# Kernel optimization log

Measured on AMD Instinct MI355X. Metric: run time of the kernel, lower is better.

The kernel has to match this reference:

```python
import jax, jax.numpy as jnp
import numpy as np


def setup_inputs() -> dict:
    key = jax.random.key(0)
    ks = jax.random.split(key, 9)
    B, Q, K, F, C = 16, 2048, 2048, 128, 2
    q = jax.random.normal(ks[0], (B, Q, F), dtype=jnp.float32)
    k = jax.random.normal(ks[1], (B, K, F), dtype=jnp.float32)
    v = jax.random.normal(ks[2], (B, K, F), dtype=jnp.float32)
    coords_q = jax.random.uniform(ks[3], (B, Q, C), dtype=jnp.float32)
    coords_k = jax.random.uniform(ks[4], (B, K, C), dtype=jnp.float32)
    attn_mask = jax.random.randint(ks[5], (B, Q, K), 0, 2).astype(jnp.bool_)
    alibi_mask = jax.random.randint(ks[6], (B, Q, K), 0, 2).astype(jnp.bool_)
    bias_scale = jax.random.uniform(ks[7], (1,), dtype=jnp.float32)  # nn.Parameter(torch.rand(1))
    running_mean = jnp.ones((1,), dtype=jnp.float32)  # RunningMeanScaler buffer (eval mode)
    return {"q": q, "k": k, "v": v, "coords_q": coords_q, "coords_k": coords_k,
            "attn_mask": attn_mask, "alibi_mask": alibi_mask,
            "bias_scale": bias_scale, "running_mean": running_mean}


def reference(q, k, v, coords_q, coords_k, attn_mask, alibi_mask, bias_scale, running_mean):
    # [b,q,k] attention logits
    scale = jnp.asarray(k.shape[-1], q.dtype) ** -0.5
    weight_logits = jnp.einsum('bqf,bkf->bqk', q, k) * scale
    # pairwise coordinate distances [b,q,k]
    diff = coords_q[:, :, None, :] - coords_k[:, None, :, :]
    distances = jnp.sqrt(jnp.sum(diff * diff, axis=-1))
    scaled_distances = (distances / running_mean) * bias_scale  # broadcast scalars
    masked_distances = jnp.where(alibi_mask, jnp.zeros((), distances.dtype), scaled_distances)
    weights = jax.nn.softmax(weight_logits, axis=-1)
    masked = jnp.where(attn_mask, jnp.zeros((), weights.dtype), weights - masked_distances)
    attention = jnp.einsum('bqk,bkf->bqf', masked, v)
    return attention
```

## Files before the change

kernel.cpp:

```cpp
#include <hip/hip_runtime.h>
#include <stdint.h>

#define B_  16
#define QL  2048
#define KL  2048
#define FD  128
#define BQ  64
#define BK  32
#define NSTEP (KL/BK)

#define KSTR  136
#define VTOFF 4352
#define VTSTR 36
#define BUFS  8960
#define WS_HALF (B_*KL*FD)

typedef __attribute__((ext_vector_type(8))) short bf16x8;
typedef __attribute__((ext_vector_type(4))) float f32x4;
typedef __attribute__((ext_vector_type(4))) int   i32x4;
typedef __attribute__((ext_vector_type(4))) unsigned int u32x4;

__device__ __forceinline__ unsigned short f2b(float f) {
  union { float f; unsigned u; } x; x.f = f;
  return (unsigned short)((x.u + 0x8000u) >> 16);
}

__device__ __forceinline__ unsigned cvt_pk_bf16(float lo, float hi) {
  unsigned r;
  asm("v_cvt_pk_bf16_f32 %0, %1, %2" : "=v"(r) : "v"(lo), "v"(hi));
  return r;
}

__global__ __launch_bounds__(256) void conv_k(const float* __restrict__ kp,
                                              unsigned short* __restrict__ kb) {
  int idx = (blockIdx.x * 256 + threadIdx.x) * 4;
  float4 u = *(const float4*)(kp + idx);
  ushort4 s4; s4.x = f2b(u.x); s4.y = f2b(u.y); s4.z = f2b(u.z); s4.w = f2b(u.w);
  *(ushort4*)(kb + idx) = s4;
}

__global__ __launch_bounds__(256) void conv_vt(const float* __restrict__ vp,
                                               unsigned short* __restrict__ vt) {
  __shared__ float tl[32 * 132];
  const int t = threadIdx.x, b = blockIdx.x >> 6, kt = blockIdx.x & 63;
  const int r = t >> 3, f0 = (t & 7) * 16;
  const float* src = vp + ((long long)(b * KL + kt * 32 + r)) * FD + f0;
  #pragma unroll
  for (int i = 0; i < 4; ++i)
    *(float4*)&tl[r * 132 + f0 + 4 * i] = *(const float4*)(src + 4 * i);
  __syncthreads();
  const int f = t >> 1, half = t & 1;
  bf16x8 o0, o1;
  #pragma unroll
  for (int j = 0; j < 8; ++j)  o0[j] = (short)f2b(tl[(half * 16 + j) * 132 + f]);
  #pragma unroll
  for (int j = 0; j < 8; ++j)  o1[j] = (short)f2b(tl[(half * 16 + 8 + j) * 132 + f]);
  unsigned short* dst = vt + ((long long)((b * 64 + kt) * FD + f)) * 32 + half * 16;
  *(bf16x8*)dst = o0;
  *(bf16x8*)(dst + 8) = o1;
}

__global__ __launch_bounds__(256, 2) void alibi_attn(
    const unsigned short* __restrict__ kbp,
    const unsigned short* __restrict__ vtp,
    const float* __restrict__ qp,
    const float* __restrict__ cqp,
    const float* __restrict__ ckp,
    const int* __restrict__ amp,
    const int* __restrict__ almp,
    const float* __restrict__ bsp,
    const float* __restrict__ rmp,
    float* __restrict__ outp)
{
  __shared__ unsigned short kv[2 * BUFS];

  const int t    = threadIdx.x;
  const int w    = t >> 6;
  const int lane = t & 63;
  const int l15  = lane & 15;
  const int q4   = lane >> 4;

  const int bid  = blockIdx.x;
  const int xcd  = bid & 7, slot = bid >> 3;
  const int b    = (xcd << 1) | (slot >> 5);
  const int qbase = (slot & 31) * BQ;

  const float bscale = bsp[0] / rmp[0];
  const float sl2 = 0.08838834764831845f * 1.44269504089f;

  const int kr_st = t >> 3, kc_st = (t & 7) * 16;
  const int vf_st = t >> 1, vh_st = (t & 1) * 16;

  {
    const float* qg = qp + ((long long)(b * QL + qbase)) * FD;
    #pragma unroll
    for (int i = 0; i < 8; ++i) {
      int idx = t + 256 * i;
      float4 u = ((const float4*)qg)[idx];
      int row = idx >> 5, col = (idx & 31) * 4;
      ushort4 s4; s4.x = f2b(u.x); s4.y = f2b(u.y); s4.z = f2b(u.z); s4.w = f2b(u.w);
      *(ushort4*)&kv[row * KSTR + col] = s4;
    }
  }
  __syncthreads();
  bf16x8 qfrag[4];
  {
    const int m = w * 16 + l15;
    #pragma unroll
    for (int fs = 0; fs < 4; ++fs)
      qfrag[fs] = *(const bf16x8*)&kv[m * KSTR + fs * 32 + q4 * 8];
  }
  const int qrow = qbase + w * 16 + l15;
  float cqx, cqy;
  {
    float2 c2 = *(const float2*)(cqp + ((long long)(b * QL + qrow)) * 2);
    cqx = c2.x; cqy = c2.y;
  }
  const long long mrow = (long long)(b * QL + qrow) * KL;
  __syncthreads();

  const unsigned short* kgb = kbp + (long long)b * KL * FD;
  const unsigned short* vgb = vtp + (long long)b * KL * FD;

  i32x4 amv[2][2], alv[2][2];
  f32x4 ckf[2][2][2];
  bf16x8 kreg[2][2], vreg[2][2];
  const int klane0 = 4 * q4;
  #pragma unroll
  for (int s = 0; s < 2; ++s) {
    const int k0 = s * 16 + klane0;
    amv[0][s] = __builtin_nontemporal_load((const i32x4*)(amp + mrow + k0));
    alv[0][s] = __builtin_nontemporal_load((const i32x4*)(almp + mrow + k0));
    ckf[0][s][0] = *(const f32x4*)(ckp + ((long long)(b * KL + k0)) * 2);
    ckf[0][s][1] = *(const f32x4*)(ckp + ((long long)(b * KL + k0)) * 2 + 4);
  }
  {
    bf16x8 k0l = *(const bf16x8*)(kgb + kr_st * FD + kc_st);
    bf16x8 k1l = *(const bf16x8*)(kgb + kr_st * FD + kc_st + 8);
    bf16x8 v0l = *(const bf16x8*)(vgb + t * 16);
    bf16x8 v1l = *(const bf16x8*)(vgb + t * 16 + 8);
    *(bf16x8*)&kv[kr_st * KSTR + kc_st]     = k0l;
    *(bf16x8*)&kv[kr_st * KSTR + kc_st + 8] = k1l;
    *(bf16x8*)&kv[VTOFF + vf_st * VTSTR + vh_st]     = v0l;
    *(bf16x8*)&kv[VTOFF + vf_st * VTSTR + vh_st + 8] = v1l;
    kreg[1][0] = *(const bf16x8*)(kgb + (BK + kr_st) * FD + kc_st);
    kreg[1][1] = *(const bf16x8*)(kgb + (BK + kr_st) * FD + kc_st + 8);
    vreg[1][0] = *(const bf16x8*)(vgb + BK * FD + t * 16);
    vreg[1][1] = *(const bf16x8*)(vgb + BK * FD + t * 16 + 8);
  }
  __syncthreads();

  f32x4 O1[8], O2[8];
  #pragma unroll
  for (int n = 0; n < 8; ++n) {
    O1[n] = (f32x4){0.f, 0.f, 0.f, 0.f};
    O2[n] = (f32x4){0.f, 0.f, 0.f, 0.f};
  }
  float lsum = 0.f;

  const int srcA = l15 + ((q4 & 1) << 5);
  const int srcB = srcA + 16;
  const bool lowhalf = (q4 < 2);

  #pragma unroll 2
  for (int kt = 0; kt < NSTEP; ++kt) {
    const int cur = kt & 1, nxt = cur ^ 1;
    const unsigned short* kb = kv + cur * BUFS;
    unsigned short*       nb = kv + nxt * BUFS;

    const int ktf = (kt + 2 < NSTEP) ? (kt + 2) : (NSTEP - 1);
    kreg[cur][0] = *(const bf16x8*)(kgb + (ktf * BK + kr_st) * FD + kc_st);
    kreg[cur][1] = *(const bf16x8*)(kgb + (ktf * BK + kr_st) * FD + kc_st + 8);
    vreg[cur][0] = *(const bf16x8*)(vgb + ktf * (BK * FD) + t * 16);
    vreg[cur][1] = *(const bf16x8*)(vgb + ktf * (BK * FD) + t * 16 + 8);

    const int ktm = (kt + 1 < NSTEP) ? (kt + 1) : kt;
    #pragma unroll
    for (int s = 0; s < 2; ++s) {
      const int kg = ktm * BK + s * 16 + klane0;
      amv[nxt][s] = __builtin_nontemporal_load((const i32x4*)(amp + mrow + kg));
      alv[nxt][s] = __builtin_nontemporal_load((const i32x4*)(almp + mrow + kg));
      ckf[nxt][s][0] = *(const f32x4*)(ckp + ((long long)(b * KL + kg)) * 2);
      ckf[nxt][s][1] = *(const f32x4*)(ckp + ((long long)(b * KL + kg)) * 2 + 4);
    }

    f32x4 S0 = (f32x4){0.f, 0.f, 0.f, 0.f};
    f32x4 S1 = (f32x4){0.f, 0.f, 0.f, 0.f};
    #pragma unroll
    for (int fs = 0; fs < 4; ++fs) {
      bf16x8 kb0 = *(const bf16x8*)&kb[(l15)      * KSTR + fs * 32 + q4 * 8];
      bf16x8 kb1 = *(const bf16x8*)&kb[(16 + l15) * KSTR + fs * 32 + q4 * 8];
      S0 = __builtin_amdgcn_mfma_f32_16x16x32_bf16(kb0, qfrag[fs], S0, 0, 0, 0);
      S1 = __builtin_amdgcn_mfma_f32_16x16x32_bf16(kb1, qfrag[fs], S1, 0, 0, 0);
    }

    float wvv[2][4], tvv[2][4];
    #pragma unroll
    for (int s = 0; s < 2; ++s) {
      const f32x4 Sv = s ? S1 : S0;
      #pragma unroll
      for (int r = 0; r < 4; ++r) {
        float e = __builtin_amdgcn_exp2f(Sv[r] * sl2);
        lsum += e;
        const float ckx = ckf[cur][s][r >> 1][(r & 1) * 2];
        const float cky = ckf[cur][s][r >> 1][(r & 1) * 2 + 1];
        float dx = cqx - ckx, dy = cqy - cky;
        float d  = sqrtf(fmaf(dx, dx, dy * dy)) * bscale;
        int am = amv[cur][s][r], al = alv[cur][s][r];
        wvv[s][r] = am ? 0.f : e;
        tvv[s][r] = (am | al) ? 0.f : d;
      }
    }

    unsigned aX0 = cvt_pk_bf16(wvv[0][0], wvv[0][1]);
    unsigned aX1 = cvt_pk_bf16(wvv[0][2], wvv[0][3]);
    unsigned aX2 = cvt_pk_bf16(wvv[1][0], wvv[1][1]);
    unsigned aX3 = cvt_pk_bf16(wvv[1][2], wvv[1][3]);
    unsigned tX0 = cvt_pk_bf16(tvv[0][0], tvv[0][1]);
    unsigned tX1 = cvt_pk_bf16(tvv[0][2], tvv[0][3]);
    unsigned tX2 = cvt_pk_bf16(tvv[1][0], tvv[1][1]);
    unsigned tX3 = cvt_pk_bf16(tvv[1][2], tvv[1][3]);

    u32x4 wa, ta;
    {
      int y0, y2;
      y0 = __shfl((int)aX0, srcA); y2 = __shfl((int)aX2, srcA);
      wa[0] = (unsigned)(lowhalf ? y0 : y2);
      y0 = __shfl((int)aX1, srcA); y2 = __shfl((int)aX3, srcA);
      wa[1] = (unsigned)(lowhalf ? y0 : y2);
      y0 = __shfl((int)aX0, srcB); y2 = __shfl((int)aX2, srcB);
      wa[2] = (unsigned)(lowhalf ? y0 : y2);
      y0 = __shfl((int)aX1, srcB); y2 = __shfl((int)aX3, srcB);
      wa[3] = (unsigned)(lowhalf ? y0 : y2);
      y0 = __shfl((int)tX0, srcA); y2 = __shfl((int)tX2, srcA);
      ta[0] = (unsigned)(lowhalf ? y0 : y2);
      y0 = __shfl((int)tX1, srcA); y2 = __shfl((int)tX3, srcA);
      ta[1] = (unsigned)(lowhalf ? y0 : y2);
      y0 = __shfl((int)tX0, srcB); y2 = __shfl((int)tX2, srcB);
      ta[2] = (unsigned)(lowhalf ? y0 : y2);
      y0 = __shfl((int)tX1, srcB); y2 = __shfl((int)tX3, srcB);
      ta[3] = (unsigned)(lowhalf ? y0 : y2);
    }
    bf16x8 aw = __builtin_bit_cast(bf16x8, wa);
    bf16x8 at = __builtin_bit_cast(bf16x8, ta);

    #pragma unroll
    for (int n = 0; n < 8; ++n) {
      bf16x8 vb = *(const bf16x8*)&kb[VTOFF + (n * 16 + l15) * VTSTR + q4 * 8];
      O1[n] = __builtin_amdgcn_mfma_f32_16x16x32_bf16(aw, vb, O1[n], 0, 0, 0);
      O2[n] = __builtin_amdgcn_mfma_f32_16x16x32_bf16(at, vb, O2[n], 0, 0, 0);
    }

    *(bf16x8*)&nb[kr_st * KSTR + kc_st]     = kreg[nxt][0];
    *(bf16x8*)&nb[kr_st * KSTR + kc_st + 8] = kreg[nxt][1];
    *(bf16x8*)&nb[VTOFF + vf_st * VTSTR + vh_st]     = vreg[nxt][0];
    *(bf16x8*)&nb[VTOFF + vf_st * VTSTR + vh_st + 8] = vreg[nxt][1];

    asm volatile("s_waitcnt lgkmcnt(0)\n\ts_barrier" ::: "memory");
  }

  lsum += __shfl_xor(lsum, 16, 64);
  lsum += __shfl_xor(lsum, 32, 64);
  float linv[4];
  #pragma unroll
  for (int r = 0; r < 4; ++r) linv[r] = 1.0f / __shfl(lsum, q4 * 4 + r, 64);

  #pragma unroll
  for (int n = 0; n < 8; ++n) {
    #pragma unroll
    for (int r = 0; r < 4; ++r) {
      const int qg_ = qbase + w * 16 + q4 * 4 + r;
      const int f   = n * 16 + l15;
      float val = O1[n][r] * linv[r] - O2[n][r];
      __builtin_nontemporal_store(val, outp + ((long long)(b * QL + qg_)) * FD + f);
    }
  }
}

extern "C" void kernel_launch(void* const* d_in, const int* in_sizes, int n_in,
                              void* d_out, int out_size, void* d_ws, size_t ws_size,
                              hipStream_t stream) {
  const float* q   = (const float*)d_in[0];
  const float* k   = (const float*)d_in[1];
  const float* v   = (const float*)d_in[2];
  const float* cq  = (const float*)d_in[3];
  const float* ck  = (const float*)d_in[4];
  const int*   am  = (const int*)d_in[5];
  const int*   alm = (const int*)d_in[6];
  const float* bs  = (const float*)d_in[7];
  const float* rm  = (const float*)d_in[8];
  float*       out = (float*)d_out;

  unsigned short* kb = (unsigned short*)d_ws;
  unsigned short* vt = kb + WS_HALF;

  hipLaunchKernelGGL(conv_k,  dim3(WS_HALF / 1024), dim3(256), 0, stream, k, kb);
  hipLaunchKernelGGL(conv_vt, dim3(B_ * 64),        dim3(256), 0, stream, v, vt);

  dim3 grid(B_ * (QL / BQ));
  dim3 block(256);
  hipLaunchKernelGGL(alibi_attn, grid, block, 0, stream,
                     kb, vt, q, cq, ck, am, alm, bs, rm, out);
}
```

Measured before the change: 676.0 us.

## Split attention kernel into producer and consumer warps with LDS handoff

Doubles the block to 512 threads. Four producer waves load K/V tiles and masks, compute the masked distance bias tiles, and pack the attn mask into bit words, passing everything through LDS. Four consumer waves only run the MFMAs, exp and softmax accumulation. This is meant to take the global loads and distance math off the MFMA waves' critical path. In exchange it adds LDS traffic and barrier coupling between the two roles, and occupancy may drop with 512-thread blocks.

```diff
diff --git a/kernel.cpp b/kernel.cpp
--- a/kernel.cpp
+++ b/kernel.cpp
@@ -60,7 +60,7 @@
   *(bf16x8*)(dst + 8) = o1;
 }
 
-__global__ __launch_bounds__(256, 2) void alibi_attn(
+__global__ __launch_bounds__(512, 2) void alibi_attn(
     const unsigned short* __restrict__ kbp,
     const unsigned short* __restrict__ vtp,
     const float* __restrict__ qp,
@@ -73,25 +73,78 @@
     float* __restrict__ outp)
 {
   __shared__ unsigned short kv[2 * BUFS];
+  __shared__ u32x4 t_lds[2][256];
+  __shared__ unsigned amw_lds[2][64];
 
   const int t    = threadIdx.x;
-  const int w    = t >> 6;
   const int lane = t & 63;
   const int l15  = lane & 15;
   const int q4   = lane >> 4;
+  const bool is_prod = (t >= 256);
 
   const int bid  = blockIdx.x;
   const int xcd  = bid & 7, slot = bid >> 3;
   const int b    = (xcd << 1) | (slot >> 5);
   const int qbase = (slot & 31) * BQ;
 
+  const float sl2 = 0.08838834764831845f * 1.44269504089f;
+
+  const unsigned short* kgb = kbp + (long long)b * KL * FD;
+  const unsigned short* vgb = vtp + (long long)b * KL * FD;
+
+  const int tp = t & 255;
+  const int kr_st = tp >> 3, kc_st = (tp & 7) * 16;
+  const int vf_st = tp >> 1, vh_st = (tp & 1) * 16;
+  const int pw = (t >> 6) & 3;
+  const int mrow16 = lane >> 2, moct = lane & 3;
+  const long long mrowP = (long long)(b * QL + qbase + pw * 16 + mrow16) * KL;
+  const int qrowT = qbase + pw * 16 + l15;
   const float bscale = bsp[0] / rmp[0];
-  const float sl2 = 0.08838834764831845f * 1.44269504089f;
-
-  const int kr_st = t >> 3, kc_st = (t & 7) * 16;
-  const int vf_st = t >> 1, vh_st = (t & 1) * 16;
-
-  {
+  float cqxP = 0.f, cqyP = 0.f;
+
+  i32x4 am0[2], am1[2], al0[2], al1[2];
+  bf16x8 krg[2], vrg[2];
+
+  auto produce = [&](int sC, int sl, int tile) {
+    unsigned am8 = 0, ob8 = 0;
+    #pragma unroll
+    for (int j = 0; j < 4; ++j) {
+      am8 |= (am0[sC][j] ? 1u : 0u) << j;
+      am8 |= (am1[sC][j] ? 1u : 0u) << (4 + j);
+      ob8 |= ((am0[sC][j] | al0[sC][j]) ? 1u : 0u) << j;
+      ob8 |= ((am1[sC][j] | al1[sC][j]) ? 1u : 0u) << (4 + j);
+    }
+    unsigned pk = am8 | (ob8 << 8);
+    unsigned amw = am8 << (moct * 8);
+    amw |= (unsigned)__shfl_xor((int)amw, 1, 64);
+    amw |= (unsigned)__shfl_xor((int)amw, 2, 64);
+    if (moct == 0) amw_lds[sl][pw * 16 + mrow16] = amw;
+    unsigned pkT = (unsigned)__shfl((int)pk, 4 * l15 + q4, 64);
+    unsigned obT = (pkT >> 8) & 0xFFu;
+    const long long cb = ((long long)(b * KL + tile * BK + 8 * q4)) * 2;
+    f32x4 cc[4];
+    cc[0] = *(const f32x4*)(ckp + cb);
+    cc[1] = *(const f32x4*)(ckp + cb + 4);
+    cc[2] = *(const f32x4*)(ckp + cb + 8);
+    cc[3] = *(const f32x4*)(ckp + cb + 12);
+    float tv[8];
+    #pragma unroll
+    for (int j = 0; j < 8; ++j) {
+      float ckx = cc[j >> 1][(j & 1) * 2];
+      float cky = cc[j >> 1][(j & 1) * 2 + 1];
+      float dx = cqxP - ckx, dy = cqyP - cky;
+      float d  = sqrtf(fmaf(dx, dx, dy * dy)) * bscale;
+      tv[j] = ((obT >> j) & 1u) ? 0.f : d;
+    }
+    u32x4 ta;
+    ta[0] = cvt_pk_bf16(tv[0], tv[1]);
+    ta[1] = cvt_pk_bf16(tv[2], tv[3]);
+    ta[2] = cvt_pk_bf16(tv[4], tv[5]);
+    ta[3] = cvt_pk_bf16(tv[6], tv[7]);
+    t_lds[sl][pw * 64 + lane] = ta;
+  };
+
+  if (!is_prod) {
     const float* qg = qp + ((long long)(b * QL + qbase)) * FD;
     #pragma unroll
     for (int i = 0; i < 8; ++i) {
@@ -101,52 +154,42 @@
       ushort4 s4; s4.x = f2b(u.x); s4.y = f2b(u.y); s4.z = f2b(u.z); s4.w = f2b(u.w);
       *(ushort4*)&kv[row * KSTR + col] = s4;
     }
+  } else {
+    float2 c2 = *(const float2*)(cqp + ((long long)(b * QL + qrowT)) * 2);
+    cqxP = c2.x; cqyP = c2.y;
+    const int kg = moct * 8;
+    am0[0] = __builtin_nontemporal_load((const i32x4*)(amp + mrowP + kg));
+    am1[0] = __builtin_nontemporal_load((const i32x4*)(amp + mrowP + kg + 4));
+    al0[0] = __builtin_nontemporal_load((const i32x4*)(almp + mrowP + kg));
+    al1[0] = __builtin_nontemporal_load((const i32x4*)(almp + mrowP + kg + 4));
+    krg[0] = *(const bf16x8*)(kgb + kr_st * FD + kc_st);
+    krg[1] = *(const bf16x8*)(kgb + kr_st * FD + kc_st + 8);
+    vrg[0] = *(const bf16x8*)(vgb + tp * 16);
+    vrg[1] = *(const bf16x8*)(vgb + tp * 16 + 8);
   }
   __syncthreads();
+
   bf16x8 qfrag[4];
-  {
-    const int m = w * 16 + l15;
+  if (!is_prod) {
+    const int m = (t >> 6) * 16 + l15;
     #pragma unroll
     for (int fs = 0; fs < 4; ++fs)
       qfrag[fs] = *(const bf16x8*)&kv[m * KSTR + fs * 32 + q4 * 8];
-  }
-  const int qrow = qbase + w * 16 + l15;
-  float cqx, cqy;
-  {
-    float2 c2 = *(const float2*)(cqp + ((long long)(b * QL + qrow)) * 2);
-    cqx = c2.x; cqy = c2.y;
-  }
-  const long long mrow = (long long)(b * QL + qrow) * KL;
+  } else {
+    produce(0, 0, 0);
+    const int kg = BK + moct * 8;
+    am0[1] = __builtin_nontemporal_load((const i32x4*)(amp + mrowP + kg));
+    am1[1] = __builtin_nontemporal_load((const i32x4*)(amp + mrowP + kg + 4));
+    al0[1] = __builtin_nontemporal_load((const i32x4*)(almp + mrowP + kg));
+    al1[1] = __builtin_nontemporal_load((const i32x4*)(almp + mrowP + kg + 4));
+  }
   __syncthreads();
 
-  const unsigned short* kgb = kbp + (long long)b * KL * FD;
-  const unsigned short* vgb = vtp + (long long)b * KL * FD;
-
-  i32x4 amv[2][2], alv[2][2];
-  f32x4 ckf[2][2][2];
-  bf16x8 kreg[2][2], vreg[2][2];
-  const int klane0 = 4 * q4;
-  #pragma unroll
-  for (int s = 0; s < 2; ++s) {
-    const int k0 = s * 16 + klane0;
-    amv[0][s] = __builtin_nontemporal_load((const i32x4*)(amp + mrow + k0));
-    alv[0][s] = __builtin_nontemporal_load((const i32x4*)(almp + mrow + k0));
-    ckf[0][s][0] = *(const f32x4*)(ckp + ((long long)(b * KL + k0)) * 2);
-    ckf[0][s][1] = *(const f32x4*)(ckp + ((long long)(b * KL + k0)) * 2 + 4);
-  }
-  {
-    bf16x8 k0l = *(const bf16x8*)(kgb + kr_st * FD + kc_st);
-    bf16x8 k1l = *(const bf16x8*)(kgb + kr_st * FD + kc_st + 8);
-    bf16x8 v0l = *(const bf16x8*)(vgb + t * 16);
-    bf16x8 v1l = *(const bf16x8*)(vgb + t * 16 + 8);
-    *(bf16x8*)&kv[kr_st * KSTR + kc_st]     = k0l;
-    *(bf16x8*)&kv[kr_st * KSTR + kc_st + 8] = k1l;
-    *(bf16x8*)&kv[VTOFF + vf_st * VTSTR + vh_st]     = v0l;
-    *(bf16x8*)&kv[VTOFF + vf_st * VTSTR + vh_st + 8] = v1l;
-    kreg[1][0] = *(const bf16x8*)(kgb + (BK + kr_st) * FD + kc_st);
-    kreg[1][1] = *(const bf16x8*)(kgb + (BK + kr_st) * FD + kc_st + 8);
-    vreg[1][0] = *(const bf16x8*)(vgb + BK * FD + t * 16);
-    vreg[1][1] = *(const bf16x8*)(vgb + BK * FD + t * 16 + 8);
+  if (is_prod) {
+    *(bf16x8*)&kv[kr_st * KSTR + kc_st]     = krg[0];
+    *(bf16x8*)&kv[kr_st * KSTR + kc_st + 8] = krg[1];
+    *(bf16x8*)&kv[VTOFF + vf_st * VTSTR + vh_st]     = vrg[0];
+    *(bf16x8*)&kv[VTOFF + vf_st * VTSTR + vh_st + 8] = vrg[1];
   }
   __syncthreads();
 
@@ -163,116 +206,93 @@
   const bool lowhalf = (q4 < 2);
 
   #pragma unroll 2
-  for (int kt = 0; kt < NSTEP; ++kt) {
-    const int cur = kt & 1, nxt = cur ^ 1;
-    const unsigned short* kb = kv + cur * BUFS;
-    unsigned short*       nb = kv + nxt * BUFS;
-
-    const int ktf = (kt + 2 < NSTEP) ? (kt + 2) : (NSTEP - 1);
-    kreg[cur][0] = *(const bf16x8*)(kgb + (ktf * BK + kr_st) * FD + kc_st);
-    kreg[cur][1] = *(const bf16x8*)(kgb + (ktf * BK + kr_st) * FD + kc_st + 8);
-    vreg[cur][0] = *(const bf16x8*)(vgb + ktf * (BK * FD) + t * 16);
-    vreg[cur][1] = *(const bf16x8*)(vgb + ktf * (BK * FD) + t * 16 + 8);
-
-    const int ktm = (kt + 1 < NSTEP) ? (kt + 1) : kt;
-    #pragma unroll
-    for (int s = 0; s < 2; ++s) {
-      const int kg = ktm * BK + s * 16 + klane0;
-      amv[nxt][s] = __builtin_nontemporal_load((const i32x4*)(amp + mrow + kg));
-      alv[nxt][s] = __builtin_nontemporal_load((const i32x4*)(almp + mrow + kg));
-      ckf[nxt][s][0] = *(const f32x4*)(ckp + ((long long)(b * KL + kg)) * 2);
-      ckf[nxt][s][1] = *(const f32x4*)(ckp + ((long long)(b * KL + kg)) * 2 + 4);
-    }
-
-    f32x4 S0 = (f32x4){0.f, 0.f, 0.f, 0.f};
-    f32x4 S1 = (f32x4){0.f, 0.f, 0.f, 0.f};
-    #pragma unroll
-    for (int fs = 0; fs < 4; ++fs) {
-      bf16x8 kb0 = *(const bf16x8*)&kb[(l15)      * KSTR + fs * 32 + q4 * 8];
-      bf16x8 kb1 = *(const bf16x8*)&kb[(16 + l15) * KSTR + fs * 32 + q4 * 8];
-      S0 = __builtin_amdgcn_mfma_f32_16x16x32_bf16(kb0, qfrag[fs], S0, 0, 0, 0);
-      S1 = __builtin_amdgcn_mfma_f32_16x16x32_bf16(kb1, qfrag[fs], S1, 0, 0, 0);
-    }
-
-    float wvv[2][4], tvv[2][4];
-    #pragma unroll
-    for (int s = 0; s < 2; ++s) {
-      const f32x4 Sv = s ? S1 : S0;
+  for (int i = 0; i < NSTEP; ++i) {
+    const int cur = i & 1, nxt = cur ^ 1;
+    if (!is_prod) {
+      const unsigned short* buf = kv + cur * BUFS;
+      f32x4 S0 = (f32x4){0.f, 0.f, 0.f, 0.f};
+      f32x4 S1 = (f32x4){0.f, 0.f, 0.f, 0.f};
+      #pragma unroll
+      for (int fs = 0; fs < 4; ++fs) {
+        bf16x8 kb0 = *(const bf16x8*)&buf[(l15)      * KSTR + fs * 32 + q4 * 8];
+        bf16x8 kb1 = *(const bf16x8*)&buf[(16 + l15) * KSTR + fs * 32 + q4 * 8];
+        S0 = __builtin_amdgcn_mfma_f32_16x16x32_bf16(kb0, qfrag[fs], S0, 0, 0, 0);
+        S1 = __builtin_amdgcn_mfma_f32_16x16x32_bf16(kb1, qfrag[fs], S1, 0, 0, 0);
+      }
+      const unsigned amw = amw_lds[cur][(t >> 6) * 16 + l15];
+      float wvv[2][4];
+      #pragma unroll
+      for (int s = 0; s < 2; ++s) {
+        const f32x4 Sv = s ? S1 : S0;
+        #pragma unroll
+        for (int r = 0; r < 4; ++r) {
+          float e = __builtin_amdgcn_exp2f(Sv[r] * sl2);
+          lsum += e;
+          wvv[s][r] = ((amw >> (s * 16 + 4 * q4 + r)) & 1u) ? 0.f : e;
+        }
+      }
+      unsigned aX0 = cvt_pk_bf16(wvv[0][0], wvv[0][1]);
+      unsigned aX1 = cvt_pk_bf16(wvv[0][2], wvv[0][3]);
+      unsigned aX2 = cvt_pk_bf16(wvv[1][0], wvv[1][1]);
+      unsigned aX3 = cvt_pk_bf16(wvv[1][2], wvv[1][3]);
+      u32x4 wa;
+      {
+        int y0, y2;
+        y0 = __shfl((int)aX0, srcA, 64); y2 = __shfl((int)aX2, srcA, 64);
+        wa[0] = (unsigned)(lowhalf ? y0 : y2);
+        y0 = __shfl((int)aX1, srcA, 64); y2 = __shfl((int)aX3, srcA, 64);
+        wa[1] = (unsigned)(lowhalf ? y0 : y2);
+        y0 = __shfl((int)aX0, srcB, 64); y2 = __shfl((int)aX2, srcB, 64);
+        wa[2] = (unsigned)(lowhalf ? y0 : y2);
+        y0 = __shfl((int)aX1, srcB, 64); y2 = __shfl((int)aX3, srcB, 64);
+        wa[3] = (unsigned)(lowhalf ? y0 : y2);
+      }
+      bf16x8 aw = __builtin_bit_cast(bf16x8, wa);
+      bf16x8 at = __builtin_bit_cast(bf16x8, t_lds[cur][(t >> 6) * 64 + lane]);
+      #pragma unroll
+      for (int n = 0; n < 8; ++n) {
+        bf16x8 vb = *(const bf16x8*)&buf[VTOFF + (n * 16 + l15) * VTSTR + q4 * 8];
+        O1[n] = __builtin_amdgcn_mfma_f32_16x16x32_bf16(aw, vb, O1[n], 0, 0, 0);
+        O2[n] = __builtin_amdgcn_mfma_f32_16x16x32_bf16(at, vb, O2[n], 0, 0, 0);
+      }
+    } else {
+      const int tn = (i + 1 < NSTEP) ? (i + 1) : (NSTEP - 1);
+      const int tf = (i + 2 < NSTEP) ? (i + 2) : (NSTEP - 1);
+      krg[0] = *(const bf16x8*)(kgb + (tn * BK + kr_st) * FD + kc_st);
+      krg[1] = *(const bf16x8*)(kgb + (tn * BK + kr_st) * FD + kc_st + 8);
+      vrg[0] = *(const bf16x8*)(vgb + tn * (BK * FD) + tp * 16);
+      vrg[1] = *(const bf16x8*)(vgb + tn * (BK * FD) + tp * 16 + 8);
+      const int kg = tf * BK + moct * 8;
+      am0[cur] = __builtin_nontemporal_load((const i32x4*)(amp + mrowP + kg));
+      am1[cur] = __builtin_nontemporal_load((const i32x4*)(amp + mrowP + kg + 4));
+      al0[cur] = __builtin_nontemporal_load((const i32x4*)(almp + mrowP + kg));
+      al1[cur] = __builtin_nontemporal_load((const i32x4*)(almp + mrowP + kg + 4));
+      produce(nxt, nxt, tn);
+      unsigned short* nb = kv + nxt * BUFS;
+      *(bf16x8*)&nb[kr_st * KSTR + kc_st]     = krg[0];
+      *(bf16x8*)&nb[kr_st * KSTR + kc_st + 8] = krg[1];
+      *(bf16x8*)&nb[VTOFF + vf_st * VTSTR + vh_st]     = vrg[0];
+      *(bf16x8*)&nb[VTOFF + vf_st * VTSTR + vh_st + 8] = vrg[1];
+    }
+    asm volatile("s_waitcnt lgkmcnt(0)\n\ts_barrier" ::: "memory");
+  }
+
+  if (!is_prod) {
+    lsum += __shfl_xor(lsum, 16, 64);
+    lsum += __shfl_xor(lsum, 32, 64);
+    float linv[4];
+    #pragma unroll
+    for (int r = 0; r < 4; ++r) linv[r] = 1.0f / __shfl(lsum, q4 * 4 + r, 64);
+    const int w = t >> 6;
+    #pragma unroll
+    for (int n = 0; n < 8; ++n) {
       #pragma unroll
       for (int r = 0; r < 4; ++r) {
-        float e = __builtin_amdgcn_exp2f(Sv[r] * sl2);
-        lsum += e;
-        const float ckx = ckf[cur][s][r >> 1][(r & 1) * 2];
-        const float cky = ckf[cur][s][r >> 1][(r & 1) * 2 + 1];
-        float dx = cqx - ckx, dy = cqy - cky;
-        float d  = sqrtf(fmaf(dx, dx, dy * dy)) * bscale;
-        int am = amv[cur][s][r], al = alv[cur][s][r];
-        wvv[s][r] = am ? 0.f : e;
-        tvv[s][r] = (am | al) ? 0.f : d;
-      }
-    }
-
-    unsigned aX0 = cvt_pk_bf16(wvv[0][0], wvv[0][1]);
-    unsigned aX1 = cvt_pk_bf16(wvv[0][2], wvv[0][3]);
-    unsigned aX2 = cvt_pk_bf16(wvv[1][0], wvv[1][1]);
-    unsigned aX3 = cvt_pk_bf16(wvv[1][2], wvv[1][3]);
-    unsigned tX0 = cvt_pk_bf16(tvv[0][0], tvv[0][1]);
-    unsigned tX1 = cvt_pk_bf16(tvv[0][2], tvv[0][3]);
-    unsigned tX2 = cvt_pk_bf16(tvv[1][0], tvv[1][1]);
-    unsigned tX3 = cvt_pk_bf16(tvv[1][2], tvv[1][3]);
-
-    u32x4 wa, ta;
-    {
-      int y0, y2;
-      y0 = __shfl((int)aX0, srcA); y2 = __shfl((int)aX2, srcA);
-      wa[0] = (unsigned)(lowhalf ? y0 : y2);
-      y0 = __shfl((int)aX1, srcA); y2 = __shfl((int)aX3, srcA);
-      wa[1] = (unsigned)(lowhalf ? y0 : y2);
-      y0 = __shfl((int)aX0, srcB); y2 = __shfl((int)aX2, srcB);
-      wa[2] = (unsigned)(lowhalf ? y0 : y2);
-      y0 = __shfl((int)aX1, srcB); y2 = __shfl((int)aX3, srcB);
-      wa[3] = (unsigned)(lowhalf ? y0 : y2);
-      y0 = __shfl((int)tX0, srcA); y2 = __shfl((int)tX2, srcA);
-      ta[0] = (unsigned)(lowhalf ? y0 : y2);
-      y0 = __shfl((int)tX1, srcA); y2 = __shfl((int)tX3, srcA);
-      ta[1] = (unsigned)(lowhalf ? y0 : y2);
-      y0 = __shfl((int)tX0, srcB); y2 = __shfl((int)tX2, srcB);
-      ta[2] = (unsigned)(lowhalf ? y0 : y2);
-      y0 = __shfl((int)tX1, srcB); y2 = __shfl((int)tX3, srcB);
-      ta[3] = (unsigned)(lowhalf ? y0 : y2);
-    }
-    bf16x8 aw = __builtin_bit_cast(bf16x8, wa);
-    bf16x8 at = __builtin_bit_cast(bf16x8, ta);
-
-    #pragma unroll
-    for (int n = 0; n < 8; ++n) {
-      bf16x8 vb = *(const bf16x8*)&kb[VTOFF + (n * 16 + l15) * VTSTR + q4 * 8];
-      O1[n] = __builtin_amdgcn_mfma_f32_16x16x32_bf16(aw, vb, O1[n], 0, 0, 0);
-      O2[n] = __builtin_amdgcn_mfma_f32_16x16x32_bf16(at, vb, O2[n], 0, 0, 0);
-    }
-
-    *(bf16x8*)&nb[kr_st * KSTR + kc_st]     = kreg[nxt][0];
-    *(bf16x8*)&nb[kr_st * KSTR + kc_st + 8] = kreg[nxt][1];
-    *(bf16x8*)&nb[VTOFF + vf_st * VTSTR + vh_st]     = vreg[nxt][0];
-    *(bf16x8*)&nb[VTOFF + vf_st * VTSTR + vh_st + 8] = vreg[nxt][1];
-
-    asm volatile("s_waitcnt lgkmcnt(0)\n\ts_barrier" ::: "memory");
-  }
-
-  lsum += __shfl_xor(lsum, 16, 64);
-  lsum += __shfl_xor(lsum, 32, 64);
-  float linv[4];
-  #pragma unroll
-  for (int r = 0; r < 4; ++r) linv[r] = 1.0f / __shfl(lsum, q4 * 4 + r, 64);
-
-  #pragma unroll
-  for (int n = 0; n < 8; ++n) {
-    #pragma unroll
-    for (int r = 0; r < 4; ++r) {
-      const int qg_ = qbase + w * 16 + q4 * 4 + r;
-      const int f   = n * 16 + l15;
-      float val = O1[n][r] * linv[r] - O2[n][r];
-      __builtin_nontemporal_store(val, outp + ((long long)(b * QL + qg_)) * FD + f);
+        const int qg_ = qbase + w * 16 + q4 * 4 + r;
+        const int f   = n * 16 + l15;
+        float val = O1[n][r] * linv[r] - O2[n][r];
+        __builtin_nontemporal_store(val, outp + ((long long)(b * QL + qg_)) * FD + f);
+      }
     }
   }
 }
@@ -298,7 +318,7 @@
   hipLaunchKernelGGL(conv_vt, dim3(B_ * 64),        dim3(256), 0, stream, v, vt);
 
   dim3 grid(B_ * (QL / BQ));
-  dim3 block(256);
+  dim3 block(512);
   hipLaunchKernelGGL(alibi_attn, grid, block, 0, stream,
                      kb, vt, q, cq, ck, am, alm, bs, rm, out);
 }
```

New measurement: 692.2 us. 1.02x slower.

## Load K/V MFMA fragments directly from global into registers, drop LDS staging

Applied to the files above, without the earlier changes.

Removes the double-buffered LDS staging of K and V tiles and the per-step barrier. Each wave now loads its MFMA operand fragments for K and V^T straight from global memory (L2-cached) into registers, prefetching one step ahead. Mask prefetch depth is raised to two steps. This trades shared-memory traffic and synchronisation for redundant global/L2 reads: all four waves in a block now fetch the same K/V data, and more registers are live, which may hurt occupancy.

```diff
diff --git a/kernel.cpp b/kernel.cpp
--- a/kernel.cpp
+++ b/kernel.cpp
@@ -10,9 +10,6 @@
 #define NSTEP (KL/BK)
 
 #define KSTR  136
-#define VTOFF 4352
-#define VTSTR 36
-#define BUFS  8960
 #define WS_HALF (B_*KL*FD)
 
 typedef __attribute__((ext_vector_type(8))) short bf16x8;
@@ -72,7 +69,7 @@
     const float* __restrict__ rmp,
     float* __restrict__ outp)
 {
-  __shared__ unsigned short kv[2 * BUFS];
+  __shared__ unsigned short qlds[BQ * KSTR];
 
   const int t    = threadIdx.x;
   const int w    = t >> 6;
@@ -87,9 +84,7 @@
 
   const float bscale = bsp[0] / rmp[0];
   const float sl2 = 0.08838834764831845f * 1.44269504089f;
-
-  const int kr_st = t >> 3, kc_st = (t & 7) * 16;
-  const int vf_st = t >> 1, vh_st = (t & 1) * 16;
+  const int klane0 = 4 * q4;
 
   {
     const float* qg = qp + ((long long)(b * QL + qbase)) * FD;
@@ -99,7 +94,7 @@
       float4 u = ((const float4*)qg)[idx];
       int row = idx >> 5, col = (idx & 31) * 4;
       ushort4 s4; s4.x = f2b(u.x); s4.y = f2b(u.y); s4.z = f2b(u.z); s4.w = f2b(u.w);
-      *(ushort4*)&kv[row * KSTR + col] = s4;
+      *(ushort4*)&qlds[row * KSTR + col] = s4;
     }
   }
   __syncthreads();
@@ -108,7 +103,7 @@
     const int m = w * 16 + l15;
     #pragma unroll
     for (int fs = 0; fs < 4; ++fs)
-      qfrag[fs] = *(const bf16x8*)&kv[m * KSTR + fs * 32 + q4 * 8];
+      qfrag[fs] = *(const bf16x8*)&qlds[m * KSTR + fs * 32 + q4 * 8];
   }
   const int qrow = qbase + w * 16 + l15;
   float cqx, cqy;
@@ -117,38 +112,31 @@
     cqx = c2.x; cqy = c2.y;
   }
   const long long mrow = (long long)(b * QL + qrow) * KL;
-  __syncthreads();
 
   const unsigned short* kgb = kbp + (long long)b * KL * FD;
   const unsigned short* vgb = vtp + (long long)b * KL * FD;
 
   i32x4 amv[2][2], alv[2][2];
   f32x4 ckf[2][2][2];
-  bf16x8 kreg[2][2], vreg[2][2];
-  const int klane0 = 4 * q4;
-  #pragma unroll
-  for (int s = 0; s < 2; ++s) {
-    const int k0 = s * 16 + klane0;
-    amv[0][s] = __builtin_nontemporal_load((const i32x4*)(amp + mrow + k0));
-    alv[0][s] = __builtin_nontemporal_load((const i32x4*)(almp + mrow + k0));
-    ckf[0][s][0] = *(const f32x4*)(ckp + ((long long)(b * KL + k0)) * 2);
-    ckf[0][s][1] = *(const f32x4*)(ckp + ((long long)(b * KL + k0)) * 2 + 4);
-  }
-  {
-    bf16x8 k0l = *(const bf16x8*)(kgb + kr_st * FD + kc_st);
-    bf16x8 k1l = *(const bf16x8*)(kgb + kr_st * FD + kc_st + 8);
-    bf16x8 v0l = *(const bf16x8*)(vgb + t * 16);
-    bf16x8 v1l = *(const bf16x8*)(vgb + t * 16 + 8);
-    *(bf16x8*)&kv[kr_st * KSTR + kc_st]     = k0l;
-    *(bf16x8*)&kv[kr_st * KSTR + kc_st + 8] = k1l;
-    *(bf16x8*)&kv[VTOFF + vf_st * VTSTR + vh_st]     = v0l;
-    *(bf16x8*)&kv[VTOFF + vf_st * VTSTR + vh_st + 8] = v1l;
-    kreg[1][0] = *(const bf16x8*)(kgb + (BK + kr_st) * FD + kc_st);
-    kreg[1][1] = *(const bf16x8*)(kgb + (BK + kr_st) * FD + kc_st + 8);
-    vreg[1][0] = *(const bf16x8*)(vgb + BK * FD + t * 16);
-    vreg[1][1] = *(const bf16x8*)(vgb + BK * FD + t * 16 + 8);
-  }
-  __syncthreads();
+  #pragma unroll
+  for (int p = 0; p < 2; ++p)
+    #pragma unroll
+    for (int s = 0; s < 2; ++s) {
+      const int kg = p * BK + s * 16 + klane0;
+      amv[p][s] = __builtin_nontemporal_load((const i32x4*)(amp + mrow + kg));
+      alv[p][s] = __builtin_nontemporal_load((const i32x4*)(almp + mrow + kg));
+      ckf[p][s][0] = *(const f32x4*)(ckp + ((long long)(b * KL + kg)) * 2);
+      ckf[p][s][1] = *(const f32x4*)(ckp + ((long long)(b * KL + kg)) * 2 + 4);
+    }
+  bf16x8 kf[8], vf[8];
+  #pragma unroll
+  for (int fs = 0; fs < 4; ++fs) {
+    kf[2 * fs]     = *(const bf16x8*)(kgb + (l15)      * FD + fs * 32 + q4 * 8);
+    kf[2 * fs + 1] = *(const bf16x8*)(kgb + (16 + l15) * FD + fs * 32 + q4 * 8);
+  }
+  #pragma unroll
+  for (int n = 0; n < 8; ++n)
+    vf[n] = *(const bf16x8*)(vgb + (n * 16 + l15) * 32 + q4 * 8);
 
   f32x4 O1[8], O2[8];
   #pragma unroll
@@ -164,34 +152,21 @@
 
   #pragma unroll 2
   for (int kt = 0; kt < NSTEP; ++kt) {
-    const int cur = kt & 1, nxt = cur ^ 1;
-    const unsigned short* kb = kv + cur * BUFS;
-    unsigned short*       nb = kv + nxt * BUFS;
-
-    const int ktf = (kt + 2 < NSTEP) ? (kt + 2) : (NSTEP - 1);
-    kreg[cur][0] = *(const bf16x8*)(kgb + (ktf * BK + kr_st) * FD + kc_st);
-    kreg[cur][1] = *(const bf16x8*)(kgb + (ktf * BK + kr_st) * FD + kc_st + 8);
-    vreg[cur][0] = *(const bf16x8*)(vgb + ktf * (BK * FD) + t * 16);
-    vreg[cur][1] = *(const bf16x8*)(vgb + ktf * (BK * FD) + t * 16 + 8);
-
-    const int ktm = (kt + 1 < NSTEP) ? (kt + 1) : kt;
-    #pragma unroll
-    for (int s = 0; s < 2; ++s) {
-      const int kg = ktm * BK + s * 16 + klane0;
-      amv[nxt][s] = __builtin_nontemporal_load((const i32x4*)(amp + mrow + kg));
-      alv[nxt][s] = __builtin_nontemporal_load((const i32x4*)(almp + mrow + kg));
-      ckf[nxt][s][0] = *(const f32x4*)(ckp + ((long long)(b * KL + kg)) * 2);
-      ckf[nxt][s][1] = *(const f32x4*)(ckp + ((long long)(b * KL + kg)) * 2 + 4);
-    }
+    const int cur = kt & 1;
+    const int kn  = (kt + 1 < NSTEP) ? (kt + 1) : kt;
+    const int kf2 = (kt + 2 < NSTEP) ? (kt + 2) : kt;
 
     f32x4 S0 = (f32x4){0.f, 0.f, 0.f, 0.f};
     f32x4 S1 = (f32x4){0.f, 0.f, 0.f, 0.f};
     #pragma unroll
     for (int fs = 0; fs < 4; ++fs) {
-      bf16x8 kb0 = *(const bf16x8*)&kb[(l15)      * KSTR + fs * 32 + q4 * 8];
-      bf16x8 kb1 = *(const bf16x8*)&kb[(16 + l15) * KSTR + fs * 32 + q4 * 8];
-      S0 = __builtin_amdgcn_mfma_f32_16x16x32_bf16(kb0, qfrag[fs], S0, 0, 0, 0);
-      S1 = __builtin_amdgcn_mfma_f32_16x16x32_bf16(kb1, qfrag[fs], S1, 0, 0, 0);
+      S0 = __builtin_amdgcn_mfma_f32_16x16x32_bf16(kf[2 * fs],     qfrag[fs], S0, 0, 0, 0);
+      S1 = __builtin_amdgcn_mfma_f32_16x16x32_bf16(kf[2 * fs + 1], qfrag[fs], S1, 0, 0, 0);
+    }
+    #pragma unroll
+    for (int fs = 0; fs < 4; ++fs) {
+      kf[2 * fs]     = *(const bf16x8*)(kgb + (kn * BK + l15)      * FD + fs * 32 + q4 * 8);
+      kf[2 * fs + 1] = *(const bf16x8*)(kgb + (kn * BK + 16 + l15) * FD + fs * 32 + q4 * 8);
     }
 
     float wvv[2][4], tvv[2][4];
@@ -211,6 +186,14 @@
         tvv[s][r] = (am | al) ? 0.f : d;
       }
     }
+    #pragma unroll
+    for (int s = 0; s < 2; ++s) {
+      const int kg = kf2 * BK + s * 16 + klane0;
+      amv[cur][s] = __builtin_nontemporal_load((const i32x4*)(amp + mrow + kg));
+      alv[cur][s] = __builtin_nontemporal_load((const i32x4*)(almp + mrow + kg));
+      ckf[cur][s][0] = *(const f32x4*)(ckp + ((long long)(b * KL + kg)) * 2);
+      ckf[cur][s][1] = *(const f32x4*)(ckp + ((long long)(b * KL + kg)) * 2 + 4);
+    }
 
     unsigned aX0 = cvt_pk_bf16(wvv[0][0], wvv[0][1]);
     unsigned aX1 = cvt_pk_bf16(wvv[0][2], wvv[0][3]);
@@ -224,21 +207,21 @@
     u32x4 wa, ta;
     {
       int y0, y2;
-      y0 = __shfl((int)aX0, srcA); y2 = __shfl((int)aX2, srcA);
+      y0 = __shfl((int)aX0, srcA, 64); y2 = __shfl((int)aX2, srcA, 64);
       wa[0] = (unsigned)(lowhalf ? y0 : y2);
-      y0 = __shfl((int)aX1, srcA); y2 = __shfl((int)aX3, srcA);
+      y0 = __shfl((int)aX1, srcA, 64); y2 = __shfl((int)aX3, srcA, 64);
       wa[1] = (unsigned)(lowhalf ? y0 : y2);
-      y0 = __shfl((int)aX0, srcB); y2 = __shfl((int)aX2, srcB);
+      y0 = __shfl((int)aX0, srcB, 64); y2 = __shfl((int)aX2, srcB, 64);
       wa[2] = (unsigned)(lowhalf ? y0 : y2);
-      y0 = __shfl((int)aX1, srcB); y2 = __shfl((int)aX3, srcB);
+      y0 = __shfl((int)aX1, srcB, 64); y2 = __shfl((int)aX3, srcB, 64);
       wa[3] = (unsigned)(lowhalf ? y0 : y2);
-      y0 = __shfl((int)tX0, srcA); y2 = __shfl((int)tX2, srcA);
+      y0 = __shfl((int)tX0, srcA, 64); y2 = __shfl((int)tX2, srcA, 64);
       ta[0] = (unsigned)(lowhalf ? y0 : y2);
-      y0 = __shfl((int)tX1, srcA); y2 = __shfl((int)tX3, srcA);
+      y0 = __shfl((int)tX1, srcA, 64); y2 = __shfl((int)tX3, srcA, 64);
       ta[1] = (unsigned)(lowhalf ? y0 : y2);
-      y0 = __shfl((int)tX0, srcB); y2 = __shfl((int)tX2, srcB);
+      y0 = __shfl((int)tX0, srcB, 64); y2 = __shfl((int)tX2, srcB, 64);
       ta[2] = (unsigned)(lowhalf ? y0 : y2);
-      y0 = __shfl((int)tX1, srcB); y2 = __shfl((int)tX3, srcB);
+      y0 = __shfl((int)tX1, srcB, 64); y2 = __shfl((int)tX3, srcB, 64);
       ta[3] = (unsigned)(lowhalf ? y0 : y2);
     }
     bf16x8 aw = __builtin_bit_cast(bf16x8, wa);
@@ -246,17 +229,12 @@
 
     #pragma unroll
     for (int n = 0; n < 8; ++n) {
-      bf16x8 vb = *(const bf16x8*)&kb[VTOFF + (n * 16 + l15) * VTSTR + q4 * 8];
-      O1[n] = __builtin_amdgcn_mfma_f32_16x16x32_bf16(aw, vb, O1[n], 0, 0, 0);
-      O2[n] = __builtin_amdgcn_mfma_f32_16x16x32_bf16(at, vb, O2[n], 0, 0, 0);
-    }
-
-    *(bf16x8*)&nb[kr_st * KSTR + kc_st]     = kreg[nxt][0];
-    *(bf16x8*)&nb[kr_st * KSTR + kc_st + 8] = kreg[nxt][1];
-    *(bf16x8*)&nb[VTOFF + vf_st * VTSTR + vh_st]     = vreg[nxt][0];
-    *(bf16x8*)&nb[VTOFF + vf_st * VTSTR + vh_st + 8] = vreg[nxt][1];
-
-    asm volatile("s_waitcnt lgkmcnt(0)\n\ts_barrier" ::: "memory");
+      O1[n] = __builtin_amdgcn_mfma_f32_16x16x32_bf16(aw, vf[n], O1[n], 0, 0, 0);
+      O2[n] = __builtin_amdgcn_mfma_f32_16x16x32_bf16(at, vf[n], O2[n], 0, 0, 0);
+    }
+    #pragma unroll
+    for (int n = 0; n < 8; ++n)
+      vf[n] = *(const bf16x8*)(vgb + (kn * FD + n * 16 + l15) * 32 + q4 * 8);
   }
 
   lsum += __shfl_xor(lsum, 16, 64);
```

After: 748.7 us. 10.7% more time.
